# Optimization experiments

Hardware: AMD Instinct MI355X
Metric: run time of the kernel (lower is better)

The kernel has to match this reference:

```python
import jax, jax.numpy as jnp
import numpy as np
import math

B, SEQ, E, H, NB, NHYP = 4, 1024, 512, 8, 64, 6
V, HID, NC, ENC = 32000, 2048, 6, 6
DH = E // H


def _pos_encoding(n, e, dtype):
    pos = jnp.arange(n, dtype=dtype)[:, None]
    div = jnp.exp(-jnp.arange(0, e, 2, dtype=dtype) * (math.log(10000.0) / e))
    ang = pos * div  # [n, e/2]
    pe = jnp.zeros((n, e), dtype)
    pe = pe.at[:, 0::2].set(jnp.sin(ang))
    pe = pe.at[:, 1::2].set(jnp.cos(ang))
    return pe


def _layer_norm(x, g, b):
    m = x.mean(-1, keepdims=True)
    v = ((x - m) ** 2).mean(-1, keepdims=True)
    return (x - m) / jnp.sqrt(v + 1e-5) * g + b


def _lsh_attention(x, Wq, bq, Wv, bv, hyper):
    b, n, e = x.shape
    q = x @ Wq + bq
    v = x @ Wv + bv
    q4 = q.reshape(b, n, H, DH)  # [b,n,h,d]
    v4 = v.reshape(b, n, H, DH)
    # bucket hashing: append bias 1, project on hyperplanes, binarize, binary-encode
    aug = jnp.concatenate([q4, jnp.ones((b, n, H, 1), q.dtype)], axis=-1)
    proj = jnp.einsum('bnhe,ey->bnhy', aug, hyper)
    bits = (proj >= 0).astype(q.dtype)
    pows = (2 ** jnp.arange(NHYP)).astype(q.dtype)
    buckets = jnp.einsum('bnhy,y->bnh', bits, pows).astype(jnp.int32)
    bh = buckets.transpose(0, 2, 1)  # [b,h,n]
    qh = q4.transpose(0, 2, 1, 3)  # [b,h,n,d]
    vh = v4.transpose(0, 2, 1, 3)
    scores = jnp.einsum('bhnd,bhmd->bhnm', qh, qh) / math.sqrt(e)
    # torch code zeroes q rows at their OWN bucket and sums q_c @ q_c^T over all
    # NB buckets; that equals scores * (NB - 2 + [bucket_i == bucket_j]) exactly.
    same = bh[:, :, :, None] == bh[:, :, None, :]
    count = (NB - 2 + same.astype(jnp.int32)).astype(scores.dtype)
    attn = jax.nn.softmax(scores * count, axis=-1)
    out = jnp.einsum('bhnm,bhmd->bhnd', attn, vh)
    return out.transpose(0, 2, 1, 3).reshape(b, n, e)


def setup_inputs() -> dict:
    key = jax.random.key(0)
    ks = jax.random.split(key, 16)
    s = 0.02
    emb = jax.random.normal(ks[0], (V, E), jnp.float32) * s
    emb = emb.at[V - 1].set(0.0)  # padding_idx row
    return dict(
        inputs=jax.random.randint(ks[1], (B, SEQ), 0, V),
        emb=emb,
        gamma=jnp.ones((E,), jnp.float32),
        beta=jnp.zeros((E,), jnp.float32),
        Wq=jax.random.normal(ks[2], (E, E), jnp.float32) * s,
        bq=jnp.zeros((E,), jnp.float32),
        Wv=jax.random.normal(ks[3], (E, E), jnp.float32) * s,
        bv=jnp.zeros((E,), jnp.float32),
        hyper=jax.random.normal(ks[4], (DH + 1, NHYP), jnp.float32),
        W1=jax.random.normal(ks[5], (E, HID), jnp.float32) * s,
        b1=jnp.zeros((HID,), jnp.float32),
        W2=jax.random.normal(ks[6], (HID, E), jnp.float32) * s,
        b2=jnp.zeros((E,), jnp.float32),
        Wm=jax.random.normal(ks[7], (E * SEQ, NC), jnp.float32) * 0.002,
        bm=jnp.zeros((NC,), jnp.float32),
    )


def reference(inputs, emb, gamma, beta, Wq, bq, Wv, bv, hyper, W1, b1, W2, b2, Wm, bm):
    x = emb[inputs]  # [B, SEQ, E]
    x = x + _pos_encoding(x.shape[1], x.shape[2], x.dtype)
    for _ in range(ENC):  # shared weights across encoders
        a = _lsh_attention(x, Wq, bq, Wv, bv, hyper)
        x = _layer_norm(a, gamma, beta)
        x = jax.nn.relu(x @ W1 + b1) @ W2 + b2 + x
        x = _layer_norm(x, gamma, beta)
    x = x.reshape(x.shape[0], -1)
    return x @ Wm + bm  # [B, NC]
```

## Files before the change

kernel.cpp:

```cpp
#include <hip/hip_runtime.h>
#include <hip/hip_bf16.h>
#include <math.h>

#define B_    4
#define SEQ_  1024
#define E_    512
#define H_    8
#define DH_   64
#define NHYP_ 6
#define HID_  2048
#define NC_   6
#define ENC_  6
#define BH_   (B_*H_)

typedef __attribute__((ext_vector_type(8))) short short8;
typedef __attribute__((ext_vector_type(4))) float f32x4;

static __device__ __forceinline__ float wave_rsum(float v){
#pragma unroll
  for(int o=32;o;o>>=1) v += __shfl_down(v,o,64);
  return v;
}
static __device__ __forceinline__ ushort f2b(float v){
  __hip_bfloat16 h = __float2bfloat16(v);
  return *(ushort*)&h;
}
static __device__ __forceinline__ void gload16(const void* g, void* l){
  __builtin_amdgcn_global_load_lds(
      (const __attribute__((address_space(1))) void*)g,
      (__attribute__((address_space(3))) void*)l,
      16, 0, 0);
}

__global__ void embed_pe_kernel(const int* __restrict__ inp, const float* __restrict__ emb,
                                float* __restrict__ x, ushort* __restrict__ xh){
  int row = blockIdx.x;
  int s = row & (SEQ_-1);
  int idx = inp[row];
  const float* er = emb + (size_t)idx*E_;
  float* xr = x + (size_t)row*E_;
  ushort* hr = xh + (size_t)row*E_;
  for(int c=threadIdx.x;c<E_;c+=blockDim.x){
    int i = c>>1;
    float div = expf(-(float)i * 0.0359778920780319646f);
    float ang = (float)s * div;
    float pe = (c&1) ? cosf(ang) : sinf(ang);
    float v = er[c] + pe;
    xr[c] = v;
    hr[c] = f2b(v);
  }
}

__global__ __launch_bounds__(256) void transpose_cast(
    const float* __restrict__ W, ushort* __restrict__ Wt, int K, int N){
  __shared__ float T[32][33];
  int tx = threadIdx.x & 31, ty = threadIdx.x >> 5;
  int n0 = blockIdx.x*32, k0 = blockIdx.y*32;
#pragma unroll
  for(int i=0;i<32;i+=8) T[ty+i][tx] = W[(size_t)(k0+ty+i)*N + n0+tx];
  __syncthreads();
#pragma unroll
  for(int i=0;i<32;i+=8)
    Wt[(size_t)(n0+ty+i)*K + k0+tx] = f2b(T[tx][ty+i]);
}

template<int BM, int BN, int EPI>
__global__ __launch_bounds__(256) void gemm_mfma(
    const ushort* __restrict__ A, const ushort* __restrict__ Bt,
    const float* __restrict__ bias, const float* __restrict__ res,
    void* __restrict__ C0, void* __restrict__ C1, int M, int N, int K)
{
  constexpr int MI = BM/32, NI = BN/32;
  constexpr int ACH = BM/32, BCH = BN/32;
  __shared__ ushort As[2][BM*64];
  __shared__ ushort Bs[2][BN*64];
  int tid = threadIdx.x;
  int w = tid>>6, lane = tid&63, g = lane>>4, li = lane&15;
  int wr = w>>1, wc = w&1;
  int bm = blockIdx.y*BM, bn = blockIdx.x*BN;
  int NK = K>>6;

  f32x4 acc[MI][NI] = {};

  auto issue = [&](int ks, int pb){
    int k0 = ks*64;
#pragma unroll
    for(int it=0; it<ACH; ++it){
      int c = it*256 + tid; int r = c>>3; int kq = ((c&7)^(r&7))*8;
      gload16(&A[(size_t)(bm+r)*K + k0 + kq], &As[pb][it*2048 + w*512]);
    }
#pragma unroll
    for(int it=0; it<BCH; ++it){
      int c = it*256 + tid; int r = c>>3; int kq = ((c&7)^(r&7))*8;
      gload16(&Bt[(size_t)(bn+r)*K + k0 + kq], &Bs[pb][it*2048 + w*512]);
    }
  };

  issue(0, 0);
  __syncthreads();
  for(int ks=0; ks<NK; ++ks){
    if(ks+1 < NK) issue(ks+1, (ks+1)&1);
    int pb = ks&1;
#pragma unroll
    for(int kc=0; kc<2; ++kc){
      short8 af[MI], bf[NI];
#pragma unroll
      for(int mi=0;mi<MI;++mi)
        af[mi] = *(const short8*)&As[pb][(wr*(BM/2)+mi*16+li)*64 + (((kc*4+g)^(li&7))*8)];
#pragma unroll
      for(int ni=0;ni<NI;++ni)
        bf[ni] = *(const short8*)&Bs[pb][(wc*(BN/2)+ni*16+li)*64 + (((kc*4+g)^(li&7))*8)];
#pragma unroll
      for(int mi=0;mi<MI;++mi)
#pragma unroll
        for(int ni=0;ni<NI;++ni)
          acc[mi][ni] = __builtin_amdgcn_mfma_f32_16x16x32_bf16(af[mi], bf[ni], acc[mi][ni], 0,0,0);
    }
    __syncthreads();
  }

#pragma unroll
  for(int mi=0;mi<MI;++mi){
    int rbase = bm + wr*(BM/2) + mi*16 + g*4;
#pragma unroll
    for(int ni=0;ni<NI;++ni){
      int cc = bn + wc*(BN/2) + ni*16 + li;
      float bv = bias[cc];
      float vv[4];
#pragma unroll
      for(int j=0;j<4;++j) vv[j] = acc[mi][ni][j] + bv;
      if(EPI==0){
#pragma unroll
        for(int j=0;j<4;++j) ((float*)C0)[(size_t)(rbase+j)*N + cc] = vv[j];
      } else if(EPI==1){
#pragma unroll
        for(int j=0;j<4;++j) ((ushort*)C0)[(size_t)(rbase+j)*N + cc] = f2b(fmaxf(vv[j],0.0f));
      } else if(EPI==2){
#pragma unroll
        for(int j=0;j<4;++j){
          size_t o = (size_t)(rbase+j)*N + cc;
          ((float*)C0)[o] = vv[j] + res[o];
        }
      } else if(EPI==3){
#pragma unroll
        for(int j=0;j<4;++j){
          int r = rbase + j;
          ((float*)C0)[(size_t)r*N + cc] = vv[j];
          int b = r>>10, n = r&1023, h = cc>>6, d = cc&63;
          ((ushort*)C1)[(((size_t)(b*8+h))*1024 + n)*64 + d] = f2b(vv[j]);
        }
      } else {
        int b = rbase>>10, n = rbase&1023, h = cc>>6, d = cc&63;
        ushort4 pk;
        pk.x = f2b(vv[0]); pk.y = f2b(vv[1]); pk.z = f2b(vv[2]); pk.w = f2b(vv[3]);
        *(ushort4*)&((ushort*)C1)[(((size_t)(b*8+h))*64 + d)*1024 + n] = pk;
      }
    }
  }
}

__global__ void bucket_kernel(const float* __restrict__ q, const float* __restrict__ hyper,
                              int* __restrict__ buckets){
  int t = blockIdx.x*256 + threadIdx.x;
  if(t >= B_*SEQ_*H_) return;
  int h = t & (H_-1);
  int n = (t >> 3) & (SEQ_-1);
  int b = t >> 13;
  const float* qr = q + ((size_t)(b*SEQ_ + n))*E_ + h*DH_;
  float pr[NHYP_];
#pragma unroll
  for(int y=0;y<NHYP_;++y) pr[y] = hyper[DH_*NHYP_ + y];
  for(int d=0;d<DH_;++d){
    float qd = qr[d];
#pragma unroll
    for(int y=0;y<NHYP_;++y) pr[y] += qd * hyper[d*NHYP_ + y];
  }
  int bk = 0;
#pragma unroll
  for(int y=0;y<NHYP_;++y) bk |= (pr[y] >= 0.0f) ? (1<<y) : 0;
  buckets[(b*H_ + h)*SEQ_ + n] = bk;
}

__global__ __launch_bounds__(256) void attn_mfma_kernel(
    const ushort* __restrict__ Qh,
    const ushort* __restrict__ Vt,
    const int* __restrict__ buckets,
    float* __restrict__ outp)
{
  int bid = blockIdx.x;
  int bh = bid & 31;
  int qt = bid >> 5;
  int b = bh >> 3, h = bh & 7;
  int tid = threadIdx.x;
  int w = tid >> 6, lane = tid & 63;
  int g = lane >> 4, li = lane & 15;

  __shared__ ushort Ks[2][64*64];
  __shared__ ushort Vs[2][64*64];
  __shared__ ushort Ps[64*68];
  __shared__ int bks[2][64];
  __shared__ int bqs[64];

  const ushort* Qbase = Qh + (size_t)bh*SEQ_*DH_;
  const ushort* Vbase = Vt + (size_t)bh*DH_*SEQ_;
  const int* Bb = buckets + bh*SEQ_;
  int q0 = qt*64;

  auto issue = [&](int kt, int pb){
    int j0 = kt*64;
#pragma unroll
    for(int it=0; it<2; ++it){
      int c = it*256 + tid; int r = c>>3; int ks = ((c&7)^(r&7))*8;
      gload16(&Qbase[(size_t)(j0+r)*DH_ + ks], &Ks[pb][it*2048 + w*512]);
      gload16(&Vbase[(size_t)r*SEQ_ + j0 + ks], &Vs[pb][it*2048 + w*512]);
    }
    if(tid < 16) gload16(&Bb[j0 + tid*4], &bks[pb][0]);
  };

  issue(0, 0);
  short8 qa[2];
  int qrow = q0 + w*16 + li;
#pragma unroll
  for(int kc=0; kc<2; ++kc)
    qa[kc] = *(const short8*)&Qbase[(size_t)qrow*DH_ + kc*32 + g*8];
  if(tid < 64) bqs[tid] = Bb[q0 + tid];
  __syncthreads();

  f32x4 acc_o[4] = {};
  float mrow[4], lrow[4];
#pragma unroll
  for(int i=0;i<4;++i){ mrow[i] = -1e30f; lrow[i] = 0.f; }

  const float invsq = 0.04419417382415922f;

  for(int kt=0; kt<16; ++kt){
    if(kt < 15) issue(kt+1, (kt+1)&1);
    int pb = kt&1;

    f32x4 accs[4];
#pragma unroll
    for(int nt=0; nt<4; ++nt){
      f32x4 z = {};
#pragma unroll
      for(int kc=0; kc<2; ++kc){
        short8 kb = *(const short8*)&Ks[pb][(nt*16+li)*64 + (((kc*4+g)^(li&7))*8)];
        z = __builtin_amdgcn_mfma_f32_16x16x32_bf16(qa[kc], kb, z, 0,0,0);
      }
      accs[nt] = z;
    }
    int bkc[4];
#pragma unroll
    for(int nt=0;nt<4;++nt) bkc[nt] = bks[pb][nt*16 + li];

    float p[4][4];
#pragma unroll
    for(int i=0;i<4;++i){
      int rloc = w*16 + g*4 + i;
      int bq = bqs[rloc];
      float rmax = -1e30f;
#pragma unroll
      for(int nt=0;nt<4;++nt){
        float cnt = (bkc[nt] == bq) ? 63.f : 62.f;
        float lg = accs[nt][i] * (invsq * cnt);
        p[nt][i] = lg;
        rmax = fmaxf(rmax, lg);
      }
#pragma unroll
      for(int o=8;o;o>>=1) rmax = fmaxf(rmax, __shfl_xor(rmax, o, 64));
      float mnew = fmaxf(mrow[i], rmax);
      float scale = __expf(mrow[i] - mnew);
      mrow[i] = mnew;
      float rs = 0.f;
#pragma unroll
      for(int nt=0;nt<4;++nt){
        float e = __expf(p[nt][i] - mnew);
        p[nt][i] = e;
        rs += e;
      }
#pragma unroll
      for(int o=8;o;o>>=1) rs += __shfl_xor(rs, o, 64);
      lrow[i] = lrow[i]*scale + rs;
#pragma unroll
      for(int dt=0;dt<4;++dt) acc_o[dt][i] *= scale;
    }
#pragma unroll
    for(int i=0;i<4;++i){
      int rloc = w*16 + g*4 + i;
#pragma unroll
      for(int nt=0;nt<4;++nt)
        Ps[rloc*68 + nt*16 + li] = f2b(p[nt][i]);
    }
#pragma unroll
    for(int dt=0; dt<4; ++dt){
      f32x4 z = acc_o[dt];
#pragma unroll
      for(int kc=0; kc<2; ++kc){
        short8 pa = *(const short8*)&Ps[(w*16+li)*68 + kc*32 + g*8];
        short8 vb = *(const short8*)&Vs[pb][(dt*16+li)*64 + (((kc*4+g)^(li&7))*8)];
        z = __builtin_amdgcn_mfma_f32_16x16x32_bf16(pa, vb, z, 0,0,0);
      }
      acc_o[dt] = z;
    }
    __syncthreads();
  }
  float* obase = outp + ((size_t)(b*SEQ_ + q0 + w*16 + g*4))*E_ + h*DH_;
#pragma unroll
  for(int i=0;i<4;++i){
    float inv = 1.0f / lrow[i];
#pragma unroll
    for(int dt=0;dt<4;++dt)
      obase[(size_t)i*E_ + dt*16 + li] = acc_o[dt][i] * inv;
  }
}

__global__ void ln_kernel(const float* __restrict__ in, const float* __restrict__ g,
                          const float* __restrict__ bb, float* __restrict__ outp,
                          ushort* __restrict__ oh){
  int row = blockIdx.x;
  const float* xr = in + (size_t)row*E_;
  float* orow = outp + (size_t)row*E_;
  ushort* hrow = oh + (size_t)row*E_;
  int tid = threadIdx.x;
  float x0 = xr[tid], x1 = xr[tid+256];
  float s = x0+x1, s2 = x0*x0 + x1*x1;
  float ws1 = wave_rsum(s);
  float ws2 = wave_rsum(s2);
  __shared__ float r1[4], r2[4];
  int w = tid>>6, lane = tid&63;
  if(lane==0){ r1[w]=ws1; r2[w]=ws2; }
  __syncthreads();
  float S  = r1[0]+r1[1]+r1[2]+r1[3];
  float S2 = r2[0]+r2[1]+r2[2]+r2[3];
  float mean = S*(1.0f/E_);
  float var  = S2*(1.0f/E_) - mean*mean;
  float inv = rsqrtf(var + 1e-5f);
  float y0 = (x0-mean)*inv*g[tid]     + bb[tid];
  float y1 = (x1-mean)*inv*g[tid+256] + bb[tid+256];
  orow[tid]     = y0;  hrow[tid]     = f2b(y0);
  orow[tid+256] = y1;  hrow[tid+256] = f2b(y1);
}

__global__ void final_partial(const float* __restrict__ x, const float* __restrict__ Wm,
                              float* __restrict__ part){
  int b  = blockIdx.x >> 7;
  int ch = blockIdx.x & 127;
  const float* xb = x + (size_t)b*SEQ_*E_;
  int k0 = ch*4096;
  float acc[NC_] = {};
  for(int k=k0+threadIdx.x; k<k0+4096; k+=256){
    float xv = xb[k];
    const float* wrow = Wm + (size_t)k*NC_;
#pragma unroll
    for(int c=0;c<NC_;++c) acc[c] += xv*wrow[c];
  }
#pragma unroll
  for(int c=0;c<NC_;++c) acc[c] = wave_rsum(acc[c]);
  __shared__ float r[4][NC_];
  int w = threadIdx.x>>6, lane = threadIdx.x&63;
  if(lane==0){
#pragma unroll
    for(int c=0;c<NC_;++c) r[w][c] = acc[c];
  }
  __syncthreads();
  if(threadIdx.x==0){
#pragma unroll
    for(int c=0;c<NC_;++c)
      part[(size_t)blockIdx.x*NC_ + c] = r[0][c]+r[1][c]+r[2][c]+r[3][c];
  }
}

__global__ void final_reduce(const float* __restrict__ part, const float* __restrict__ bm,
                             float* __restrict__ out){
  int t = threadIdx.x;
  if(t >= B_*NC_) return;
  int b = t / NC_, c = t % NC_;
  float s = bm[c];
  for(int i=0;i<128;++i) s += part[(size_t)(b*128+i)*NC_ + c];
  out[t] = s;
}

extern "C" void kernel_launch(void* const* d_in, const int* in_sizes, int n_in,
                              void* d_out, int out_size, void* d_ws, size_t ws_size,
                              hipStream_t stream){
  const int*   inp   = (const int*)d_in[0];
  const float* emb   = (const float*)d_in[1];
  const float* gamma = (const float*)d_in[2];
  const float* beta  = (const float*)d_in[3];
  const float* Wq    = (const float*)d_in[4];
  const float* bq    = (const float*)d_in[5];
  const float* Wv    = (const float*)d_in[6];
  const float* bv    = (const float*)d_in[7];
  const float* hyper = (const float*)d_in[8];
  const float* W1    = (const float*)d_in[9];
  const float* b1    = (const float*)d_in[10];
  const float* W2    = (const float*)d_in[11];
  const float* b2    = (const float*)d_in[12];
  const float* Wm    = (const float*)d_in[13];
  const float* bm    = (const float*)d_in[14];
  float* out = (float*)d_out;

  char* ws = (char*)d_ws;
  size_t off = 0;
  auto alloc = [&](size_t bytes)->void*{
    void* p = ws + off; off += (bytes + 255) & ~(size_t)255; return p;
  };
  const size_t NTOK = (size_t)B_*SEQ_;
  float*  X   = (float*)alloc(NTOK*E_*sizeof(float));
  float*  Q   = (float*)alloc(NTOK*E_*sizeof(float));
  float*  A   = (float*)alloc(NTOK*E_*sizeof(float));
  ushort* Xh  = (ushort*)alloc(NTOK*E_*sizeof(ushort));
  ushort* Hh  = (ushort*)alloc(NTOK*HID_*sizeof(ushort));
  int*    Bk  = (int*)  alloc((size_t)BH_*SEQ_*sizeof(int));
  float*  Pp  = (float*)alloc((size_t)B_*128*NC_*sizeof(float));
  ushort* Qh  = (ushort*)alloc((size_t)BH_*SEQ_*DH_*sizeof(ushort));
  ushort* Vt  = (ushort*)alloc((size_t)BH_*DH_*SEQ_*sizeof(ushort));
  ushort* WqT = (ushort*)alloc((size_t)E_*E_*sizeof(ushort));
  ushort* WvT = (ushort*)alloc((size_t)E_*E_*sizeof(ushort));
  ushort* W1T = (ushort*)alloc((size_t)HID_*E_*sizeof(ushort));
  ushort* W2T = (ushort*)alloc((size_t)E_*HID_*sizeof(ushort));
  (void)ws_size; (void)in_sizes; (void)n_in; (void)out_size;

  transpose_cast<<<dim3(E_/32,  E_/32),  256, 0, stream>>>(Wq, WqT, E_, E_);
  transpose_cast<<<dim3(E_/32,  E_/32),  256, 0, stream>>>(Wv, WvT, E_, E_);
  transpose_cast<<<dim3(HID_/32,E_/32),  256, 0, stream>>>(W1, W1T, E_, HID_);
  transpose_cast<<<dim3(E_/32,  HID_/32),256, 0, stream>>>(W2, W2T, HID_, E_);

  embed_pe_kernel<<<B_*SEQ_, 256, 0, stream>>>(inp, emb, X, Xh);

  dim3 gQV(E_/64,    (B_*SEQ_)/64);
  dim3 gF1(HID_/128, (B_*SEQ_)/128);
  dim3 gF2(E_/64,    (B_*SEQ_)/64);
  for(int l=0;l<ENC_;++l){
    gemm_mfma<64,64,3><<<gQV, 256, 0, stream>>>(Xh, WqT, bq, nullptr, Q, Qh, B_*SEQ_, E_, E_);
    gemm_mfma<64,64,4><<<gQV, 256, 0, stream>>>(Xh, WvT, bv, nullptr, nullptr, Vt, B_*SEQ_, E_, E_);
    bucket_kernel<<<(B_*SEQ_*H_)/256, 256, 0, stream>>>(Q, hyper, Bk);
    attn_mfma_kernel<<<BH_*16, 256, 0, stream>>>(Qh, Vt, Bk, A);
    ln_kernel<<<B_*SEQ_, 256, 0, stream>>>(A, gamma, beta, X, Xh);
    gemm_mfma<128,128,1><<<gF1, 256, 0, stream>>>(Xh, W1T, b1, nullptr, Hh, nullptr, B_*SEQ_, HID_, E_);
    gemm_mfma<64,64,2><<<gF2, 256, 0, stream>>>(Hh, W2T, b2, X, A, nullptr, B_*SEQ_, E_, HID_);
    ln_kernel<<<B_*SEQ_, 256, 0, stream>>>(A, gamma, beta, X, Xh);
  }
  final_partial<<<B_*128, 256, 0, stream>>>(X, Wm, Pp);
  final_reduce<<<1, 32, 0, stream>>>(Pp, bm, out);
}
```

Before: 705.3 us.

## Fuse QV projection, use static softmax bound in attention, vectorize layernorm

Concatenates Wq and Wv so a single GEMM produces Q (fp32 and head layout) and transposed V. The bucket kernel also writes squared query norms. Attention uses these to pick a fixed per-row softmax offset from a Cauchy-Schwarz bound, removing online max tracking, rescaling and per-tile shuffles. LayerNorm processes one row per wave with float4 loads, and s_setprio hints wrap the MFMA sections. The fixed offset risks exponent underflow if the bound is loose.

```diff
diff --git a/kernel.cpp b/kernel.cpp
--- a/kernel.cpp
+++ b/kernel.cpp
@@ -64,11 +64,19 @@
     Wt[(size_t)(n0+ty+i)*K + k0+tx] = f2b(T[tx][ty+i]);
 }
 
+__global__ void concat_bias(const float* __restrict__ a, const float* __restrict__ b,
+                            float* __restrict__ o){
+  int t = threadIdx.x + blockIdx.x*256;
+  if(t < 512) o[t] = a[t];
+  else if(t < 1024) o[t] = b[t-512];
+}
+
 template<int BM, int BN, int EPI>
 __global__ __launch_bounds__(256) void gemm_mfma(
     const ushort* __restrict__ A, const ushort* __restrict__ Bt,
     const float* __restrict__ bias, const float* __restrict__ res,
-    void* __restrict__ C0, void* __restrict__ C1, int M, int N, int K)
+    void* __restrict__ C0, void* __restrict__ C1, void* __restrict__ C2,
+    int M, int N, int K)
 {
   constexpr int MI = BM/32, NI = BN/32;
   constexpr int ACH = BM/32, BCH = BN/32;
@@ -141,26 +149,30 @@
           size_t o = (size_t)(rbase+j)*N + cc;
           ((float*)C0)[o] = vv[j] + res[o];
         }
-      } else if(EPI==3){
-#pragma unroll
-        for(int j=0;j<4;++j){
-          int r = rbase + j;
-          ((float*)C0)[(size_t)r*N + cc] = vv[j];
-          int b = r>>10, n = r&1023, h = cc>>6, d = cc&63;
-          ((ushort*)C1)[(((size_t)(b*8+h))*1024 + n)*64 + d] = f2b(vv[j]);
+      } else {
+        if(cc < 512){
+          int h = cc>>6, d = cc&63;
+#pragma unroll
+          for(int j=0;j<4;++j){
+            int r = rbase + j;
+            ((float*)C0)[(size_t)r*512 + cc] = vv[j];
+            int b = r>>10, n = r&1023;
+            ((ushort*)C1)[(((size_t)(b*8+h))*1024 + n)*64 + d] = f2b(vv[j]);
+          }
+        } else {
+          int cl = cc - 512; int h = cl>>6, d = cl&63;
+          int b = rbase>>10, n = rbase&1023;
+          ushort4 pk;
+          pk.x = f2b(vv[0]); pk.y = f2b(vv[1]); pk.z = f2b(vv[2]); pk.w = f2b(vv[3]);
+          *(ushort4*)&((ushort*)C2)[(((size_t)(b*8+h))*64 + d)*1024 + n] = pk;
         }
-      } else {
-        int b = rbase>>10, n = rbase&1023, h = cc>>6, d = cc&63;
-        ushort4 pk;
-        pk.x = f2b(vv[0]); pk.y = f2b(vv[1]); pk.z = f2b(vv[2]); pk.w = f2b(vv[3]);
-        *(ushort4*)&((ushort*)C1)[(((size_t)(b*8+h))*64 + d)*1024 + n] = pk;
       }
     }
   }
 }
 
 __global__ void bucket_kernel(const float* __restrict__ q, const float* __restrict__ hyper,
-                              int* __restrict__ buckets){
+                              int* __restrict__ buckets, float* __restrict__ qn2){
   int t = blockIdx.x*256 + threadIdx.x;
   if(t >= B_*SEQ_*H_) return;
   int h = t & (H_-1);
@@ -170,21 +182,26 @@
   float pr[NHYP_];
 #pragma unroll
   for(int y=0;y<NHYP_;++y) pr[y] = hyper[DH_*NHYP_ + y];
+  float s2 = 0.f;
   for(int d=0;d<DH_;++d){
     float qd = qr[d];
+    s2 += qd*qd;
 #pragma unroll
     for(int y=0;y<NHYP_;++y) pr[y] += qd * hyper[d*NHYP_ + y];
   }
   int bk = 0;
 #pragma unroll
   for(int y=0;y<NHYP_;++y) bk |= (pr[y] >= 0.0f) ? (1<<y) : 0;
-  buckets[(b*H_ + h)*SEQ_ + n] = bk;
+  int o = (b*H_ + h)*SEQ_ + n;
+  buckets[o] = bk;
+  qn2[o] = s2;
 }
 
 __global__ __launch_bounds__(256) void attn_mfma_kernel(
     const ushort* __restrict__ Qh,
     const ushort* __restrict__ Vt,
     const int* __restrict__ buckets,
+    const float* __restrict__ qn2,
     float* __restrict__ outp)
 {
   int bid = blockIdx.x;
@@ -200,10 +217,12 @@
   __shared__ ushort Ps[64*68];
   __shared__ int bks[2][64];
   __shared__ int bqs[64];
+  __shared__ float mred[4];
 
   const ushort* Qbase = Qh + (size_t)bh*SEQ_*DH_;
   const ushort* Vbase = Vt + (size_t)bh*DH_*SEQ_;
   const int* Bb = buckets + bh*SEQ_;
+  const float* qn = qn2 + bh*SEQ_;
   int q0 = qt*64;
 
   auto issue = [&](int kt, int pb){
@@ -224,20 +243,31 @@
   for(int kc=0; kc<2; ++kc)
     qa[kc] = *(const short8*)&Qbase[(size_t)qrow*DH_ + kc*32 + g*8];
   if(tid < 64) bqs[tid] = Bb[q0 + tid];
+
+  float mx = 0.f;
+  for(int i=tid;i<SEQ_;i+=256) mx = fmaxf(mx, qn[i]);
+#pragma unroll
+  for(int o=32;o;o>>=1) mx = fmaxf(mx, __shfl_xor(mx, o, 64));
+  if(lane==0) mred[w] = mx;
   __syncthreads();
+  float maxn = sqrtf(fmaxf(fmaxf(mred[0],mred[1]), fmaxf(mred[2],mred[3])));
+
+  const float invsq = 0.04419417382415922f;
+  const float c63 = invsq * 63.0f;
+  float Mrow[4];
+#pragma unroll
+  for(int i=0;i<4;++i)
+    Mrow[i] = c63 * sqrtf(qn[q0 + w*16 + g*4 + i]) * maxn + 1.0f;
 
   f32x4 acc_o[4] = {};
-  float mrow[4], lrow[4];
-#pragma unroll
-  for(int i=0;i<4;++i){ mrow[i] = -1e30f; lrow[i] = 0.f; }
-
-  const float invsq = 0.04419417382415922f;
+  float psum[4] = {0.f,0.f,0.f,0.f};
 
   for(int kt=0; kt<16; ++kt){
     if(kt < 15) issue(kt+1, (kt+1)&1);
     int pb = kt&1;
 
     f32x4 accs[4];
+    __builtin_amdgcn_s_setprio(1);
 #pragma unroll
     for(int nt=0; nt<4; ++nt){
       f32x4 z = {};
@@ -248,48 +278,26 @@
       }
       accs[nt] = z;
     }
+    __builtin_amdgcn_s_setprio(0);
     int bkc[4];
 #pragma unroll
     for(int nt=0;nt<4;++nt) bkc[nt] = bks[pb][nt*16 + li];
 
-    float p[4][4];
 #pragma unroll
     for(int i=0;i<4;++i){
       int rloc = w*16 + g*4 + i;
       int bq = bqs[rloc];
-      float rmax = -1e30f;
+      float rs = 0.f;
 #pragma unroll
       for(int nt=0;nt<4;++nt){
         float cnt = (bkc[nt] == bq) ? 63.f : 62.f;
-        float lg = accs[nt][i] * (invsq * cnt);
-        p[nt][i] = lg;
-        rmax = fmaxf(rmax, lg);
+        float e = __expf(accs[nt][i] * (invsq * cnt) - Mrow[i]);
+        rs += e;
+        Ps[rloc*68 + nt*16 + li] = f2b(e);
       }
-#pragma unroll
-      for(int o=8;o;o>>=1) rmax = fmaxf(rmax, __shfl_xor(rmax, o, 64));
-      float mnew = fmaxf(mrow[i], rmax);
-      float scale = __expf(mrow[i] - mnew);
-      mrow[i] = mnew;
-      float rs = 0.f;
-#pragma unroll
-      for(int nt=0;nt<4;++nt){
-        float e = __expf(p[nt][i] - mnew);
-        p[nt][i] = e;
-        rs += e;
-      }
-#pragma unroll
-      for(int o=8;o;o>>=1) rs += __shfl_xor(rs, o, 64);
-      lrow[i] = lrow[i]*scale + rs;
-#pragma unroll
-      for(int dt=0;dt<4;++dt) acc_o[dt][i] *= scale;
-    }
-#pragma unroll
-    for(int i=0;i<4;++i){
-      int rloc = w*16 + g*4 + i;
-#pragma unroll
-      for(int nt=0;nt<4;++nt)
-        Ps[rloc*68 + nt*16 + li] = f2b(p[nt][i]);
-    }
+      psum[i] += rs;
+    }
+    __builtin_amdgcn_s_setprio(1);
 #pragma unroll
     for(int dt=0; dt<4; ++dt){
       f32x4 z = acc_o[dt];
@@ -301,43 +309,54 @@
       }
       acc_o[dt] = z;
     }
+    __builtin_amdgcn_s_setprio(0);
     __syncthreads();
   }
+#pragma unroll
+  for(int i=0;i<4;++i){
+#pragma unroll
+    for(int o=8;o;o>>=1) psum[i] += __shfl_xor(psum[i], o, 64);
+  }
   float* obase = outp + ((size_t)(b*SEQ_ + q0 + w*16 + g*4))*E_ + h*DH_;
 #pragma unroll
   for(int i=0;i<4;++i){
-    float inv = 1.0f / lrow[i];
+    float inv = 1.0f / fmaxf(psum[i], 1e-35f);
 #pragma unroll
     for(int dt=0;dt<4;++dt)
       obase[(size_t)i*E_ + dt*16 + li] = acc_o[dt][i] * inv;
   }
 }
 
-__global__ void ln_kernel(const float* __restrict__ in, const float* __restrict__ g,
-                          const float* __restrict__ bb, float* __restrict__ outp,
-                          ushort* __restrict__ oh){
-  int row = blockIdx.x;
-  const float* xr = in + (size_t)row*E_;
-  float* orow = outp + (size_t)row*E_;
-  ushort* hrow = oh + (size_t)row*E_;
-  int tid = threadIdx.x;
-  float x0 = xr[tid], x1 = xr[tid+256];
-  float s = x0+x1, s2 = x0*x0 + x1*x1;
-  float ws1 = wave_rsum(s);
-  float ws2 = wave_rsum(s2);
-  __shared__ float r1[4], r2[4];
-  int w = tid>>6, lane = tid&63;
-  if(lane==0){ r1[w]=ws1; r2[w]=ws2; }
-  __syncthreads();
-  float S  = r1[0]+r1[1]+r1[2]+r1[3];
-  float S2 = r2[0]+r2[1]+r2[2]+r2[3];
-  float mean = S*(1.0f/E_);
-  float var  = S2*(1.0f/E_) - mean*mean;
+__global__ __launch_bounds__(256) void ln_kernel(
+    const float* __restrict__ in, const float* __restrict__ g,
+    const float* __restrict__ bb, float* __restrict__ outp,
+    ushort* __restrict__ oh){
+  int row = blockIdx.x*4 + (threadIdx.x>>6);
+  int lane = threadIdx.x & 63;
+  const float4* xr = (const float4*)(in + (size_t)row*E_);
+  float4 v0 = xr[lane*2], v1 = xr[lane*2+1];
+  float s  = v0.x+v0.y+v0.z+v0.w + v1.x+v1.y+v1.z+v1.w;
+  float s2 = v0.x*v0.x+v0.y*v0.y+v0.z*v0.z+v0.w*v0.w
+           + v1.x*v1.x+v1.y*v1.y+v1.z*v1.z+v1.w*v1.w;
+#pragma unroll
+  for(int o=32;o;o>>=1){ s += __shfl_xor(s,o,64); s2 += __shfl_xor(s2,o,64); }
+  float mean = s*(1.0f/E_);
+  float var  = s2*(1.0f/E_) - mean*mean;
   float inv = rsqrtf(var + 1e-5f);
-  float y0 = (x0-mean)*inv*g[tid]     + bb[tid];
-  float y1 = (x1-mean)*inv*g[tid+256] + bb[tid+256];
-  orow[tid]     = y0;  hrow[tid]     = f2b(y0);
-  orow[tid+256] = y1;  hrow[tid+256] = f2b(y1);
+  const float4* g4 = (const float4*)(g) + lane*2;
+  const float4* b4 = (const float4*)(bb) + lane*2;
+  float4 g0 = g4[0], g1 = g4[1], b0 = b4[0], b1 = b4[1];
+  float4 y0, y1;
+  y0.x=(v0.x-mean)*inv*g0.x+b0.x; y0.y=(v0.y-mean)*inv*g0.y+b0.y;
+  y0.z=(v0.z-mean)*inv*g0.z+b0.z; y0.w=(v0.w-mean)*inv*g0.w+b0.w;
+  y1.x=(v1.x-mean)*inv*g1.x+b1.x; y1.y=(v1.y-mean)*inv*g1.y+b1.y;
+  y1.z=(v1.z-mean)*inv*g1.z+b1.z; y1.w=(v1.w-mean)*inv*g1.w+b1.w;
+  float4* orow = (float4*)(outp + (size_t)row*E_) + lane*2;
+  orow[0] = y0; orow[1] = y1;
+  ushort hs[8];
+  hs[0]=f2b(y0.x); hs[1]=f2b(y0.y); hs[2]=f2b(y0.z); hs[3]=f2b(y0.w);
+  hs[4]=f2b(y1.x); hs[5]=f2b(y1.y); hs[6]=f2b(y1.z); hs[7]=f2b(y1.w);
+  *(uint4*)&oh[(size_t)row*E_ + lane*8] = *(uint4*)hs;
 }
 
 __global__ void final_partial(const float* __restrict__ x, const float* __restrict__ Wm,
@@ -405,40 +424,41 @@
     void* p = ws + off; off += (bytes + 255) & ~(size_t)255; return p;
   };
   const size_t NTOK = (size_t)B_*SEQ_;
-  float*  X   = (float*)alloc(NTOK*E_*sizeof(float));
-  float*  Q   = (float*)alloc(NTOK*E_*sizeof(float));
-  float*  A   = (float*)alloc(NTOK*E_*sizeof(float));
-  ushort* Xh  = (ushort*)alloc(NTOK*E_*sizeof(ushort));
-  ushort* Hh  = (ushort*)alloc(NTOK*HID_*sizeof(ushort));
-  int*    Bk  = (int*)  alloc((size_t)BH_*SEQ_*sizeof(int));
-  float*  Pp  = (float*)alloc((size_t)B_*128*NC_*sizeof(float));
-  ushort* Qh  = (ushort*)alloc((size_t)BH_*SEQ_*DH_*sizeof(ushort));
-  ushort* Vt  = (ushort*)alloc((size_t)BH_*DH_*SEQ_*sizeof(ushort));
-  ushort* WqT = (ushort*)alloc((size_t)E_*E_*sizeof(ushort));
-  ushort* WvT = (ushort*)alloc((size_t)E_*E_*sizeof(ushort));
-  ushort* W1T = (ushort*)alloc((size_t)HID_*E_*sizeof(ushort));
-  ushort* W2T = (ushort*)alloc((size_t)E_*HID_*sizeof(ushort));
+  float*  X    = (float*)alloc(NTOK*E_*sizeof(float));
+  float*  Q    = (float*)alloc(NTOK*E_*sizeof(float));
+  float*  A    = (float*)alloc(NTOK*E_*sizeof(float));
+  ushort* Xh   = (ushort*)alloc(NTOK*E_*sizeof(ushort));
+  ushort* Hh   = (ushort*)alloc(NTOK*HID_*sizeof(ushort));
+  int*    Bk   = (int*)  alloc((size_t)BH_*SEQ_*sizeof(int));
+  float*  Qn2  = (float*)alloc((size_t)BH_*SEQ_*sizeof(float));
+  float*  Pp   = (float*)alloc((size_t)B_*128*NC_*sizeof(float));
+  ushort* Qh   = (ushort*)alloc((size_t)BH_*SEQ_*DH_*sizeof(ushort));
+  ushort* Vt   = (ushort*)alloc((size_t)BH_*DH_*SEQ_*sizeof(ushort));
+  ushort* WqvT = (ushort*)alloc((size_t)1024*E_*sizeof(ushort));
+  ushort* W1T  = (ushort*)alloc((size_t)HID_*E_*sizeof(ushort));
+  ushort* W2T  = (ushort*)alloc((size_t)E_*HID_*sizeof(ushort));
+  float*  bqv  = (float*)alloc(1024*sizeof(float));
   (void)ws_size; (void)in_sizes; (void)n_in; (void)out_size;
 
-  transpose_cast<<<dim3(E_/32,  E_/32),  256, 0, stream>>>(Wq, WqT, E_, E_);
-  transpose_cast<<<dim3(E_/32,  E_/32),  256, 0, stream>>>(Wv, WvT, E_, E_);
+  transpose_cast<<<dim3(E_/32,  E_/32),  256, 0, stream>>>(Wq, WqvT, E_, E_);
+  transpose_cast<<<dim3(E_/32,  E_/32),  256, 0, stream>>>(Wv, WqvT + (size_t)512*E_, E_, E_);
   transpose_cast<<<dim3(HID_/32,E_/32),  256, 0, stream>>>(W1, W1T, E_, HID_);
   transpose_cast<<<dim3(E_/32,  HID_/32),256, 0, stream>>>(W2, W2T, HID_, E_);
+  concat_bias<<<4, 256, 0, stream>>>(bq, bv, bqv);
 
   embed_pe_kernel<<<B_*SEQ_, 256, 0, stream>>>(inp, emb, X, Xh);
 
-  dim3 gQV(E_/64,    (B_*SEQ_)/64);
+  dim3 gQV(1024/64,  (B_*SEQ_)/64);
   dim3 gF1(HID_/128, (B_*SEQ_)/128);
   dim3 gF2(E_/64,    (B_*SEQ_)/64);
   for(int l=0;l<ENC_;++l){
-    gemm_mfma<64,64,3><<<gQV, 256, 0, stream>>>(Xh, WqT, bq, nullptr, Q, Qh, B_*SEQ_, E_, E_);
-    gemm_mfma<64,64,4><<<gQV, 256, 0, stream>>>(Xh, WvT, bv, nullptr, nullptr, Vt, B_*SEQ_, E_, E_);
-    bucket_kernel<<<(B_*SEQ_*H_)/256, 256, 0, stream>>>(Q, hyper, Bk);
-    attn_mfma_kernel<<<BH_*16, 256, 0, stream>>>(Qh, Vt, Bk, A);
-    ln_kernel<<<B_*SEQ_, 256, 0, stream>>>(A, gamma, beta, X, Xh);
-    gemm_mfma<128,128,1><<<gF1, 256, 0, stream>>>(Xh, W1T, b1, nullptr, Hh, nullptr, B_*SEQ_, HID_, E_);
-    gemm_mfma<64,64,2><<<gF2, 256, 0, stream>>>(Hh, W2T, b2, X, A, nullptr, B_*SEQ_, E_, HID_);
-    ln_kernel<<<B_*SEQ_, 256, 0, stream>>>(A, gamma, beta, X, Xh);
+    gemm_mfma<64,64,5><<<gQV, 256, 0, stream>>>(Xh, WqvT, bqv, nullptr, Q, Qh, Vt, B_*SEQ_, 1024, E_);
+    bucket_kernel<<<(B_*SEQ_*H_)/256, 256, 0, stream>>>(Q, hyper, Bk, Qn2);
+    attn_mfma_kernel<<<BH_*16, 256, 0, stream>>>(Qh, Vt, Bk, Qn2, A);
+    ln_kernel<<<B_*SEQ_/4, 256, 0, stream>>>(A, gamma, beta, X, Xh);
+    gemm_mfma<128,128,1><<<gF1, 256, 0, stream>>>(Xh, W1T, b1, nullptr, Hh, nullptr, nullptr, B_*SEQ_, HID_, E_);
+    gemm_mfma<64,64,2><<<gF2, 256, 0, stream>>>(Hh, W2T, b2, X, A, nullptr, nullptr, B_*SEQ_, E_, HID_);
+    ln_kernel<<<B_*SEQ_/4, 256, 0, stream>>>(A, gamma, beta, X, Xh);
   }
   final_partial<<<B_*128, 256, 0, stream>>>(X, Wm, Pp);
   final_reduce<<<1, 32, 0, stream>>>(Pp, bm, out);
```

Result: faster. 599.4 us (median of 2 runs) (-15.0%).
